# Kernel optimization log

Measured on AMD Instinct MI355X. Metric: run time of the kernel, lower is better.

The kernel has to match this reference:

```python
import jax, jax.numpy as jnp
import numpy as np

N = 50000       # nodes
E = 1600000     # edges (avg degree 32)
D = 128         # h_dim
R = 20          # num_rels = 2 * n_labels
L = 2           # RelGraphConv layers (2*n_layers // 2)


def setup_inputs() -> dict:
    key = jax.random.key(0)
    ks = jax.random.split(key, 7)
    node_embeddings = jax.random.normal(ks[0], (N, D), dtype=jnp.float32)
    edge_src = jax.random.randint(ks[1], (E,), 0, N, dtype=jnp.int32)
    edge_dst = jax.random.randint(ks[2], (E,), 0, N, dtype=jnp.int32)
    etypes = jax.random.randint(ks[3], (E,), 0, R, dtype=jnp.int32)
    # per-layer learned params (DGL RelGraphConv, regularizer=None):
    # W: per-relation weight [L, R, D, D]; loop_w: self-loop weight; bias.
    W = jax.random.normal(ks[4], (L, R, D, D), dtype=jnp.float32) / np.float32(np.sqrt(D))
    loop_w = jax.random.normal(ks[5], (L, D, D), dtype=jnp.float32) / np.float32(np.sqrt(D))
    bias = jax.random.normal(ks[6], (L, D), dtype=jnp.float32) * 0.01
    return {
        "node_embeddings": node_embeddings,
        "W": W,
        "loop_w": loop_w,
        "bias": bias,
        "edge_src": edge_src,
        "edge_dst": edge_dst,
        "etypes": etypes,
    }


def reference(node_embeddings, W, loop_w, bias, edge_src, edge_dst, etypes):
    # Stacked RelGraphConv: msg_e = h[src_e] @ W[rel_e]; sum-scatter to dst;
    # h' = agg + h @ loop_w + bias (no activation applied in module forward).
    h = node_embeddings
    num_nodes = h.shape[0]
    for l in range(L):
        # transform every node by every relation once: [N, R, D]
        hW = jnp.einsum('ni,rio->nro', h, W[l])
        msg = hW[edge_src, etypes]                                  # [E, D] gather
        agg = jax.ops.segment_sum(msg, edge_dst, num_segments=num_nodes)
        h = agg + h @ loop_w[l] + bias[l]
    return h
```

## Files before the change

kernel.cpp:

```cpp
#include <hip/hip_runtime.h>
#include <hip/hip_bf16.h>
#include <stdint.h>


#define NN 50000
#define NE 1600000
#define DIM 128
#define NREL 20
#define NRELP 21
#define TILE 16
#define NTILE (NN / TILE)
#define CELLS (NN * NREL)
#define CHB 256
#define CHE (NE / CHB)
#define SPK_CAP 1024
#define PACKED_ELEMS (2 * NRELP * 4 * 8 * 64 * 8)
#define CVT_BLKS (NN * DIM / 4 / 256)
#define PKW_BLKS ((PACKED_ELEMS + 255) / 256)

typedef __attribute__((ext_vector_type(8))) short short8;
typedef __attribute__((ext_vector_type(8))) _Float16 half8;
typedef __attribute__((ext_vector_type(4))) float f32x4;

__device__ __forceinline__ unsigned short f32_to_f16_raw(float f) {
  union { _Float16 h; unsigned short u; } c;
  c.h = (_Float16)f;
  return c.u;
}

__global__ __launch_bounds__(256) void entry_kernel(
    const int* __restrict__ dst, unsigned int* __restrict__ cnt,
    const float* __restrict__ h0, unsigned short* __restrict__ hb0,
    const float* __restrict__ W, const float* __restrict__ loop_w,
    unsigned short* __restrict__ WP) {
  const int b = blockIdx.x;
  if (b < CHB) {
    __shared__ unsigned int h[NTILE];
    for (int i = threadIdx.x; i < NTILE; i += 256) h[i] = 0u;
    __syncthreads();
    const int base = b * CHE;
    for (int i = base + threadIdx.x; i < base + CHE; i += 256)
      atomicAdd(&h[dst[i] >> 4], 1u);
    __syncthreads();
    unsigned int* row = cnt + (size_t)b * NTILE;
    for (int i = threadIdx.x; i < NTILE; i += 256) row[i] = h[i];
  } else if (b < CHB + CVT_BLKS) {
    const int i = (b - CHB) * 256 + threadIdx.x;
    float4 f = ((const float4*)h0)[i];
    unsigned long long p =
        (unsigned long long)f32_to_f16_raw(f.x)
      | ((unsigned long long)f32_to_f16_raw(f.y) << 16)
      | ((unsigned long long)f32_to_f16_raw(f.z) << 32)
      | ((unsigned long long)f32_to_f16_raw(f.w) << 48);
    __builtin_nontemporal_store(p, (unsigned long long*)hb0 + i);
  } else {
    const int idx = (b - CHB - CVT_BLKS) * 256 + threadIdx.x;
    if (idx >= PACKED_ELEMS) return;
    int j = idx & 7;       int t = idx >> 3;
    int lane = t & 63;     t >>= 6;
    int nc = t & 7;        t >>= 3;
    int ks = t & 3;        t >>= 2;
    int r = t % NRELP;     int l = t / NRELP;
    int k = ks * 32 + (lane >> 4) * 8 + j;
    int n = nc * 16 + (lane & 15);
    float v = (r < NREL) ? W[(((size_t)l * NREL + r) * DIM + k) * DIM + n]
                         : loop_w[((size_t)l * DIM + k) * DIM + n];
    WP[idx] = f32_to_f16_raw(v);
  }
}

__global__ __launch_bounds__(256) void colscan_kernel(
    unsigned int* __restrict__ cnt, unsigned int* __restrict__ csum) {
  const int b = (blockIdx.x * 256 + threadIdx.x) >> 6;
  const int lane = threadIdx.x & 63;
  if (b >= NTILE) return;
  unsigned int v[4], p[4], s = 0;
#pragma unroll
  for (int i = 0; i < 4; ++i) {
    v[i] = cnt[(size_t)(lane * 4 + i) * NTILE + b];
    p[i] = s; s += v[i];
  }
  unsigned int run = s;
  for (int d = 1; d < 64; d <<= 1) {
    unsigned int t = __shfl_up(run, d);
    if (lane >= d) run += t;
  }
  const unsigned int excl = run - s;
#pragma unroll
  for (int i = 0; i < 4; ++i)
    cnt[(size_t)(lane * 4 + i) * NTILE + b] = excl + p[i];
  if (lane == 63) csum[b] = run;
}

__global__ __launch_bounds__(1024) void scan1_kernel(
    const unsigned int* __restrict__ csum, unsigned int* __restrict__ starts) {
  __shared__ unsigned int buf[1024];
  const int t = threadIdx.x;
  const int base = t * 4;
  unsigned int v[4], p[4], s = 0;
#pragma unroll
  for (int j = 0; j < 4; ++j) {
    v[j] = (base + j < NTILE) ? csum[base + j] : 0u;
    p[j] = s; s += v[j];
  }
  buf[t] = s;
  __syncthreads();
  for (int d = 1; d < 1024; d <<= 1) {
    unsigned int a = (t >= d) ? buf[t - d] : 0u;
    __syncthreads();
    buf[t] += a;
    __syncthreads();
  }
  unsigned int excl = buf[t] - s;
#pragma unroll
  for (int j = 0; j < 4; ++j)
    if (base + j < NTILE) starts[base + j] = excl + p[j];
  if (t == 1023) starts[NTILE] = buf[1023];
}

__global__ __launch_bounds__(256) void scatter_kernel(
    const int* __restrict__ src, const int* __restrict__ dst,
    const int* __restrict__ et, const unsigned int* __restrict__ starts,
    const unsigned int* __restrict__ cnt, unsigned int* __restrict__ ep) {
  __shared__ unsigned int cur[NTILE];
  const unsigned int* row = cnt + (size_t)blockIdx.x * NTILE;
  for (int i = threadIdx.x; i < NTILE; i += 256)
    cur[i] = starts[i] + row[i];
  __syncthreads();
  const int base = blockIdx.x * CHE;
  for (int i = base + threadIdx.x; i < base + CHE; i += 256) {
    int d = dst[i];
    unsigned int pos = atomicAdd(&cur[d >> 4], 1u);
    ep[pos] = (unsigned int)src[i] | ((unsigned int)(d & 15) << 16)
            | ((unsigned int)et[i] << 20);
  }
}

__global__ __launch_bounds__(512) void tile_sort_kernel(
    const unsigned int* __restrict__ ep, const unsigned int* __restrict__ starts,
    unsigned short* __restrict__ es, unsigned int* __restrict__ cofs) {
  __shared__ unsigned int hist[512];
  const int t = threadIdx.x;
  const int tile = blockIdx.x;
  const unsigned int start = starts[tile];
  const unsigned int end = starts[tile + 1];
  const int cnt = (int)(end - start);
  hist[t] = 0u;
  __syncthreads();
  for (int i = t; i < cnt; i += 512) {
    unsigned int p = ep[start + i];
    atomicAdd(&hist[((p >> 16) & 15u) * 20u + (p >> 20)], 1u);
  }
  __syncthreads();
  unsigned int own = hist[t];
  for (int d = 1; d < 512; d <<= 1) {
    __syncthreads();
    unsigned int a = (t >= d) ? hist[t - d] : 0u;
    __syncthreads();
    hist[t] += a;
  }
  __syncthreads();
  unsigned int excl = hist[t] - own;
  hist[t] = excl;
  if (t < 320) cofs[(size_t)tile * 320 + t] = start + excl;
  if (tile == NTILE - 1 && t == 0) cofs[CELLS] = (unsigned int)NE;
  __syncthreads();
  for (int i = t; i < cnt; i += 512) {
    unsigned int p = ep[start + i];
    int sub = (int)(((p >> 16) & 15u) * 20u + (p >> 20));
    unsigned int rk = atomicAdd(&hist[sub], 1u);
    es[start + rk] = (unsigned short)(p & 0xffffu);
  }
}

__global__ __launch_bounds__(512, 8) void rgcn_layer_kernel(
    const unsigned short* __restrict__ hb,
    const unsigned short* __restrict__ WP,
    const float* __restrict__ bias,
    int layer,
    const unsigned int* __restrict__ cofs,
    const unsigned short* __restrict__ es,
    float* __restrict__ outf,
    unsigned short* __restrict__ outb)
{
  __shared__ half8 Sb8[TILE * 80];
  __shared__ unsigned int cofs_l[321];
  __shared__ unsigned short spk[SPK_CAP];

  const int tid  = threadIdx.x;
  const int lane = tid & 63;
  const int w    = tid >> 6;
  const int quad = lane >> 4;
  const int m    = lane & 15;
  const int mh8  = m * 8;
  const int half = w >> 2;
  const int g    = (w & 3) * 4 + quad;
  const int dst_base = blockIdx.x * TILE;

  for (int i = tid; i < 321; i += 512) cofs_l[i] = cofs[blockIdx.x * (TILE * NREL) + i];
  __syncthreads();
  const int e0 = (int)cofs_l[0];
  const int etot = (int)cofs_l[320] - e0;
  const bool use_lds = (etot <= SPK_CAP);
  if (use_lds)
    for (int i = tid; i < etot; i += 512) spk[i] = es[e0 + i];
  __syncthreads();

  f32x4 acc = (f32x4){0.f, 0.f, 0.f, 0.f};

  for (int c = 0; c < 5; ++c) {
    if (c < 4) {
      const int cbase = g * NREL + c * 5;
      const int rlA = half ? 2 : 0;
      const int rlB = half ? 5 : 2;
      const int beg    = (int)cofs_l[cbase + rlA] - e0;
      const int endAll = (int)cofs_l[cbase + rlB] - e0;

      half8 a = (half8)(_Float16)0;
      int rl = rlA;
      int nend = (int)cofs_l[cbase + rl + 1] - e0;

      auto flush = [&]() {
        Sb8[g * 80 + ((rl * 16 + m) ^ g)] = a;
        a = (half8)(_Float16)0;
      };
      auto bump = [&](int i) {
        while (i >= nend) {
          flush();
          ++rl;
          nend = (int)cofs_l[cbase + rl + 1] - e0;
        }
      };
      auto run_walk = [&](auto fetch) {
        for (int i = beg; i < endAll; i += 6) {
          const int nrem = endAll - i;
          half8 h0, h1, h2, h3, h4, h5;
          h0 = fetch(i);
          if (nrem > 1) h1 = fetch(i + 1);
          if (nrem > 2) h2 = fetch(i + 2);
          if (nrem > 3) h3 = fetch(i + 3);
          if (nrem > 4) h4 = fetch(i + 4);
          if (nrem > 5) h5 = fetch(i + 5);
          bump(i);      a += h0;
          if (nrem > 1) { bump(i + 1); a += h1; }
          if (nrem > 2) { bump(i + 2); a += h2; }
          if (nrem > 3) { bump(i + 3); a += h3; }
          if (nrem > 4) { bump(i + 4); a += h4; }
          if (nrem > 5) { bump(i + 5); a += h5; }
        }
        while (rl < rlB) { flush(); ++rl; }
      };

      if (use_lds) {
        run_walk([&](int i) {
          return *(const half8*)(hb + (size_t)spk[i] * DIM + mh8);
        });
      } else {
        run_walk([&](int i) {
          return *(const half8*)(hb + (size_t)es[e0 + i] * DIM + mh8);
        });
      }
    } else if (half == 0) {
      half8 hv = *(const half8*)(hb + (size_t)(dst_base + g) * DIM + mh8);
      Sb8[g * 80 + (m ^ g)] = hv;
    }
    __syncthreads();

    const int rc = (c == 4) ? 1 : 5;
    for (int rl2 = 0; rl2 < rc; ++rl2) {
      const int r = (c == 4) ? (NRELP - 1) : (c * 5 + rl2);
      const unsigned short* bp =
          WP + ((((size_t)(layer * NRELP + r) * 4) * 8 + w) * 64 + lane) * 8;
#pragma unroll
      for (int ks = 0; ks < 4; ++ks) {
        half8 av = Sb8[m * 80 + ((rl2 * 16 + ks * 4 + quad) ^ m)];
        half8 bv = *(const half8*)(bp + (size_t)ks * 4096);
        acc = __builtin_amdgcn_mfma_f32_16x16x32_f16(av, bv, acc, 0, 0, 0);
      }
    }
    __syncthreads();
  }

  const int col = w * 16 + m;
  const float bv = bias[col];
  if (outb) {
#pragma unroll
    for (int i = 0; i < 4; ++i)
      outb[(size_t)(dst_base + quad * 4 + i) * DIM + col] =
          f32_to_f16_raw(acc[i] + bv);
  } else {
#pragma unroll
    for (int i = 0; i < 4; ++i)
      outf[(size_t)(dst_base + quad * 4 + i) * DIM + col] = acc[i] + bv;
  }
}

extern "C" void kernel_launch(void* const* d_in, const int* in_sizes, int n_in,
                              void* d_out, int out_size, void* d_ws, size_t ws_size,
                              hipStream_t stream) {
  const float* h0     = (const float*)d_in[0];
  const float* W      = (const float*)d_in[1];
  const float* loop_w = (const float*)d_in[2];
  const float* bias   = (const float*)d_in[3];
  const int* esrc     = (const int*)d_in[4];
  const int* edst     = (const int*)d_in[5];
  const int* etyp     = (const int*)d_in[6];
  float* out = (float*)d_out;

  char* ws = (char*)d_ws;
  size_t off = 0;
  auto alloc = [&](size_t bytes) -> void* {
    void* p = ws + off;
    off = (off + bytes + 255) & ~(size_t)255;
    return p;
  };
  unsigned short* hb0   = (unsigned short*)alloc((size_t)NN * DIM * 2);
  unsigned short* hb1   = (unsigned short*)alloc((size_t)NN * DIM * 2);
  unsigned short* WP    = (unsigned short*)alloc((size_t)PACKED_ELEMS * 2);
  unsigned int*   cnt   = (unsigned int*)alloc((size_t)CHB * NTILE * 4);
  unsigned int*   csum  = (unsigned int*)alloc((size_t)NTILE * 4);
  unsigned int*   starts= (unsigned int*)alloc((size_t)(NTILE + 1) * 4);
  unsigned int*   ep    = (unsigned int*)alloc((size_t)NE * 4);
  unsigned int*   cofs  = (unsigned int*)alloc((size_t)(CELLS + 1) * 4);
  unsigned short* es    = (unsigned short*)alloc((size_t)NE * 2);

  entry_kernel<<<CHB + CVT_BLKS + PKW_BLKS, 256, 0, stream>>>(
      edst, cnt, h0, hb0, W, loop_w, WP);
  colscan_kernel<<<(NTILE * 64 + 255) / 256, 256, 0, stream>>>(cnt, csum);
  scan1_kernel<<<1, 1024, 0, stream>>>(csum, starts);
  scatter_kernel<<<CHB, 256, 0, stream>>>(esrc, edst, etyp, starts, cnt, ep);
  tile_sort_kernel<<<NTILE, 512, 0, stream>>>(ep, starts, es, cofs);

  rgcn_layer_kernel<<<NTILE, 512, 0, stream>>>(hb0, WP, bias, 0, cofs, es,
                                               nullptr, hb1);
  rgcn_layer_kernel<<<NTILE, 512, 0, stream>>>(hb1, WP, bias + DIM, 1, cofs, es,
                                               out, nullptr);
}
```

Measured before the change: 395.1 us.

## Fuse per-tile edge sort into first RGCN layer kernel

```diff
diff --git a/kernel.cpp b/kernel.cpp
--- a/kernel.cpp
+++ b/kernel.cpp
@@ -136,56 +136,23 @@
   }
 }
 
-__global__ __launch_bounds__(512) void tile_sort_kernel(
-    const unsigned int* __restrict__ ep, const unsigned int* __restrict__ starts,
-    unsigned short* __restrict__ es, unsigned int* __restrict__ cofs) {
-  __shared__ unsigned int hist[512];
-  const int t = threadIdx.x;
-  const int tile = blockIdx.x;
-  const unsigned int start = starts[tile];
-  const unsigned int end = starts[tile + 1];
-  const int cnt = (int)(end - start);
-  hist[t] = 0u;
-  __syncthreads();
-  for (int i = t; i < cnt; i += 512) {
-    unsigned int p = ep[start + i];
-    atomicAdd(&hist[((p >> 16) & 15u) * 20u + (p >> 20)], 1u);
-  }
-  __syncthreads();
-  unsigned int own = hist[t];
-  for (int d = 1; d < 512; d <<= 1) {
-    __syncthreads();
-    unsigned int a = (t >= d) ? hist[t - d] : 0u;
-    __syncthreads();
-    hist[t] += a;
-  }
-  __syncthreads();
-  unsigned int excl = hist[t] - own;
-  hist[t] = excl;
-  if (t < 320) cofs[(size_t)tile * 320 + t] = start + excl;
-  if (tile == NTILE - 1 && t == 0) cofs[CELLS] = (unsigned int)NE;
-  __syncthreads();
-  for (int i = t; i < cnt; i += 512) {
-    unsigned int p = ep[start + i];
-    int sub = (int)(((p >> 16) & 15u) * 20u + (p >> 20));
-    unsigned int rk = atomicAdd(&hist[sub], 1u);
-    es[start + rk] = (unsigned short)(p & 0xffffu);
-  }
-}
-
 __global__ __launch_bounds__(512, 8) void rgcn_layer_kernel(
     const unsigned short* __restrict__ hb,
     const unsigned short* __restrict__ WP,
     const float* __restrict__ bias,
     int layer,
-    const unsigned int* __restrict__ cofs,
-    const unsigned short* __restrict__ es,
+    unsigned int* __restrict__ cofs,
+    unsigned short* __restrict__ es,
+    const unsigned int* __restrict__ ep,
+    const unsigned int* __restrict__ startsg,
     float* __restrict__ outf,
     unsigned short* __restrict__ outb)
 {
   __shared__ half8 Sb8[TILE * 80];
   __shared__ unsigned int cofs_l[321];
   __shared__ unsigned short spk[SPK_CAP];
+  __shared__ unsigned int esp_l[SPK_CAP];
+  __shared__ unsigned int hist[512];
 
   const int tid  = threadIdx.x;
   const int lane = tid & 63;
@@ -197,14 +164,66 @@
   const int g    = (w & 3) * 4 + quad;
   const int dst_base = blockIdx.x * TILE;
 
-  for (int i = tid; i < 321; i += 512) cofs_l[i] = cofs[blockIdx.x * (TILE * NREL) + i];
-  __syncthreads();
-  const int e0 = (int)cofs_l[0];
-  const int etot = (int)cofs_l[320] - e0;
-  const bool use_lds = (etot <= SPK_CAP);
-  if (use_lds)
-    for (int i = tid; i < etot; i += 512) spk[i] = es[e0 + i];
-  __syncthreads();
+  int e0, etot;
+  bool use_lds;
+  if (ep) {
+    const unsigned int start = startsg[blockIdx.x];
+    const unsigned int end   = startsg[blockIdx.x + 1];
+    const int cnt = (int)(end - start);
+    e0 = (int)start; etot = cnt;
+    use_lds = (cnt <= SPK_CAP);
+    hist[tid] = 0u;
+    __syncthreads();
+    if (use_lds) {
+      for (int i = tid; i < cnt; i += 512) {
+        unsigned int p = ep[start + i];
+        esp_l[i] = p;
+        atomicAdd(&hist[((p >> 16) & 15u) * 20u + (p >> 20)], 1u);
+      }
+    } else {
+      for (int i = tid; i < cnt; i += 512) {
+        unsigned int p = ep[start + i];
+        atomicAdd(&hist[((p >> 16) & 15u) * 20u + (p >> 20)], 1u);
+      }
+    }
+    __syncthreads();
+    unsigned int own = hist[tid];
+    for (int d = 1; d < 512; d <<= 1) {
+      __syncthreads();
+      unsigned int a = (tid >= d) ? hist[tid - d] : 0u;
+      __syncthreads();
+      hist[tid] += a;
+    }
+    __syncthreads();
+    unsigned int excl = hist[tid] - own;
+    hist[tid] = excl;
+    if (tid < 320) {
+      cofs_l[tid] = start + excl;
+      cofs[(size_t)blockIdx.x * 320 + tid] = start + excl;
+    }
+    if (tid == 320) cofs_l[320] = end;
+    if (blockIdx.x == NTILE - 1 && tid == 0) cofs[CELLS] = (unsigned int)NE;
+    __syncthreads();
+    for (int i = tid; i < cnt; i += 512) {
+      unsigned int p = use_lds ? esp_l[i] : ep[start + i];
+      int sub = (int)(((p >> 16) & 15u) * 20u + (p >> 20));
+      unsigned int rk = atomicAdd(&hist[sub], 1u);
+      unsigned short s = (unsigned short)(p & 0xffffu);
+      if (use_lds) spk[rk] = s;
+      es[start + rk] = s;
+    }
+    __syncthreads();
+  } else {
+    for (int i = tid; i < 321; i += 512)
+      cofs_l[i] = cofs[blockIdx.x * (TILE * NREL) + i];
+    __syncthreads();
+    e0 = (int)cofs_l[0];
+    etot = (int)cofs_l[320] - e0;
+    use_lds = (etot <= SPK_CAP);
+    if (use_lds)
+      for (int i = tid; i < etot; i += 512) spk[i] = es[e0 + i];
+    __syncthreads();
+  }
 
   f32x4 acc = (f32x4){0.f, 0.f, 0.f, 0.f};
 
@@ -329,10 +348,9 @@
   colscan_kernel<<<(NTILE * 64 + 255) / 256, 256, 0, stream>>>(cnt, csum);
   scan1_kernel<<<1, 1024, 0, stream>>>(csum, starts);
   scatter_kernel<<<CHB, 256, 0, stream>>>(esrc, edst, etyp, starts, cnt, ep);
-  tile_sort_kernel<<<NTILE, 512, 0, stream>>>(ep, starts, es, cofs);
 
   rgcn_layer_kernel<<<NTILE, 512, 0, stream>>>(hb0, WP, bias, 0, cofs, es,
-                                               nullptr, hb1);
+                                               ep, starts, nullptr, hb1);
   rgcn_layer_kernel<<<NTILE, 512, 0, stream>>>(hb1, WP, bias + DIM, 1, cofs, es,
-                                               out, nullptr);
-}
+                                               nullptr, nullptr, out, nullptr);
+}
```

Result: faster. 382.5 us, median of 2 (-3.2%).
